# Optimization experiments

Hardware: AMD Instinct MI355X
Metric: run time of the kernel (lower is better)

Reference implementation:

```python
import jax, jax.numpy as jnp
import numpy as np

B, H, W, C, NC = 4, 64, 64, 64, 19


def setup_inputs() -> dict:
    key = jax.random.key(0)
    ks = jax.random.split(key, 12)
    s = 0.05  # small init so sigmoid scores are not saturated
    return {
        "feature": jax.random.normal(ks[0], (B, H, W, C), dtype=jnp.float32),
        "predict": jax.random.normal(ks[1], (B, H, W, NC), dtype=jnp.float32),
        # height attention params (dim = H); k_linear in source is unused (q reused as k)
        "hq_w": jax.random.normal(ks[2], (H, H), dtype=jnp.float32) * s,
        "hq_b": jnp.zeros((H,), dtype=jnp.float32),
        "hv_w": jax.random.normal(ks[3], (H, H), dtype=jnp.float32) * s,
        "hv_b": jnp.zeros((H,), dtype=jnp.float32),
        # width attention params (dim = W)
        "wq_w": jax.random.normal(ks[4], (W, W), dtype=jnp.float32) * s,
        "wq_b": jnp.zeros((W,), dtype=jnp.float32),
        "wv_w": jax.random.normal(ks[5], (W, W), dtype=jnp.float32) * s,
        "wv_b": jnp.zeros((W,), dtype=jnp.float32),
        # gating scalars (nn.Parameter(torch.zeros(1)) in source; random here to exercise path)
        "h_gate": jax.random.normal(ks[6], (1,), dtype=jnp.float32) * 0.5,
        "w_gate": jax.random.normal(ks[7], (1,), dtype=jnp.float32) * 0.5,
        # 1x1 conv num_classes -> 1 (stored as [NC, 1] matrix; 1x1 conv == per-pixel linear)
        "conv_w": jax.random.normal(ks[8], (NC, 1), dtype=jnp.float32) * s,
        "conv_b": jnp.zeros((1,), dtype=jnp.float32),
    }


def _self_atten(x, wq, bq, wv, bv, dim):
    # Source uses q_linear for BOTH q and k (k_linear dead), softmax replaced by sigmoid.
    q = x @ wq + bq                                   # [B, N, dim]
    v = x @ wv + bv                                   # [B, N, dim]
    scores = jax.nn.sigmoid(jnp.einsum('bnd,bmd->bnm', q, q) / jnp.sqrt(jnp.float32(dim)))
    return jnp.einsum('bnm,bmd->bnd', scores, v)      # [B, N, dim]


def _axial(x, hq_w, hq_b, hv_w, hv_b, wq_w, wq_b, wv_w, wv_b, h_gate, w_gate):
    b, h, w, c = x.shape
    # height attention: seq = W*C, feature dim = H
    xh = x.transpose(0, 2, 3, 1).reshape(b, w * c, h)
    xh = _self_atten(xh, hq_w, hq_b, hv_w, hv_b, h)
    xh = xh.reshape(b, w, c, h).transpose(0, 3, 1, 2)  # back to [B,H,W,C]
    x = xh * h_gate + x
    # width attention: seq = H*C, feature dim = W
    xw = x.transpose(0, 1, 3, 2).reshape(b, h * c, w)
    xw = _self_atten(xw, wq_w, wq_b, wv_w, wv_b, w)
    xw = xw.reshape(b, h, c, w).transpose(0, 1, 3, 2)  # back to [B,H,W,C]
    x = xw * w_gate + x
    return x


def reference(feature, predict, hq_w, hq_b, hv_w, hv_b, wq_w, wq_b, wv_w, wv_b,
              h_gate, w_gate, conv_w, conv_b):
    feat = feature + _axial(feature, hq_w, hq_b, hv_w, hv_b,
                            wq_w, wq_b, wv_w, wv_b, h_gate, w_gate)
    p = 1.0 - jax.nn.sigmoid(predict)                 # [B,H,W,NC]
    p = p @ conv_w + conv_b                           # 1x1 conv -> [B,H,W,1]
    return p * feat                                   # broadcast gate -> [B,H,W,C]
```

## Files before the change

### kernel.cpp

```cpp
#include <hip/hip_runtime.h>

typedef _Float16 f16x8 __attribute__((ext_vector_type(8)));
typedef __fp16   fp16x2 __attribute__((ext_vector_type(2)));
typedef float f32x16 __attribute__((ext_vector_type(16)));

__device__ __forceinline__ unsigned pkrtz(float a, float b) {
    fp16x2 h = __builtin_amdgcn_cvt_pkrtz(a, b);
    union { fp16x2 h; unsigned u; } c; c.h = h; return c.u;
}

__device__ __forceinline__ unsigned short f2h(float f) {
    _Float16 h = (_Float16)f;
    union { _Float16 h; unsigned short s; } c; c.h = h; return c.s;
}

__global__ __launch_bounds__(256) void prep_kernel(
    const float* __restrict__ src,
    const float* __restrict__ wq, const float* __restrict__ bq,
    const float* __restrict__ wv, const float* __restrict__ bv,
    unsigned short* __restrict__ Qg, unsigned short* __restrict__ Vtg)
{
    __shared__ float slab[64][65];
    __shared__ float wqs[4096];
    __shared__ float wvs[4096];

    const int t  = threadIdx.x;
    const int bx = blockIdx.x, b = blockIdx.y;

    {
        const float4* wq4 = (const float4*)wq;
        const float4* wv4 = (const float4*)wv;
        float4* q4 = (float4*)wqs; float4* v4 = (float4*)wvs;
        #pragma unroll
        for (int i = 0; i < 4; ++i) {
            q4[i*256 + t] = wq4[i*256 + t];
            v4[i*256 + t] = wv4[i*256 + t];
        }
    }
    {
        const int k = t >> 2, c0 = (t & 3) << 4;
        const size_t sb = (size_t)b*262144 + (size_t)k*4096 + (size_t)bx*64 + c0;
        #pragma unroll
        for (int i = 0; i < 4; ++i)
            *(float4*)&slab[k][c0 + i*4] = *(const float4*)&src[sb + i*4];
    }
    __syncthreads();

    const int c = t & 63, jg = t >> 6;
    float qa[16], va[16];
    #pragma unroll
    for (int jj = 0; jj < 16; ++jj) { qa[jj] = bq[jg*16+jj]; va[jj] = bv[jg*16+jj]; }
    for (int k = 0; k < 64; ++k) {
        const float xv = slab[k][c];
        const float* wqr = &wqs[k*64 + jg*16];
        const float* wvr = &wvs[k*64 + jg*16];
        #pragma unroll
        for (int jj = 0; jj < 16; ++jj) {
            qa[jj] += xv * wqr[jj];
            va[jj] += xv * wvr[jj];
        }
    }
    const int token = bx*64 + c;
    union { unsigned u[8]; uint4 v[2]; } qp;
    #pragma unroll
    for (int jj = 0; jj < 8; ++jj) qp.u[jj] = pkrtz(qa[2*jj], qa[2*jj+1]);
    const size_t qoff = ((size_t)b*4096 + token)*64 + jg*16;
    *(uint4*)&Qg[qoff]     = qp.v[0];
    *(uint4*)&Qg[qoff + 8] = qp.v[1];
    #pragma unroll
    for (int jj = 0; jj < 16; ++jj)
        Vtg[((size_t)b*64 + jg*16 + jj)*4096 + token] = f2h(va[jj]);
}

__global__ __launch_bounds__(256) void prep_w_kernel(
    const float* __restrict__ feature, const float* __restrict__ Pin,
    const float* __restrict__ gate,
    const float* __restrict__ wq, const float* __restrict__ bq,
    const float* __restrict__ wv, const float* __restrict__ bv,
    unsigned short* __restrict__ Qg, unsigned short* __restrict__ Vtg,
    float* __restrict__ x1out, int nsplit)
{
    __shared__ float slab[64][65];
    __shared__ float wqs[4096];
    __shared__ float wvs[4096];

    const int t  = threadIdx.x;
    const int bx = blockIdx.x, b = blockIdx.y;

    {
        const float4* wq4 = (const float4*)wq;
        const float4* wv4 = (const float4*)wv;
        float4* q4 = (float4*)wqs; float4* v4 = (float4*)wvs;
        #pragma unroll
        for (int i = 0; i < 4; ++i) {
            q4[i*256 + t] = wq4[i*256 + t];
            v4[i*256 + t] = wv4[i*256 + t];
        }
    }
    {
        const int k = t >> 2, c0 = (t & 3) << 4;
        const size_t off = (size_t)bx*4096 + (size_t)k*64 + c0;
        const size_t fb  = (size_t)b*262144 + off;
        const float g = gate[0];
        #pragma unroll
        for (int i = 0; i < 4; ++i) {
            float4 v  = *(const float4*)&feature[fb + i*4];
            float sx = 0.f, sy = 0.f, sz = 0.f, sw = 0.f;
            for (int ks = 0; ks < nsplit; ++ks) {
                float4 pk = *(const float4*)&Pin[((size_t)(ks*4 + b) << 18) + off + i*4];
                sx += pk.x; sy += pk.y; sz += pk.z; sw += pk.w;
            }
            v.x += g * sx; v.y += g * sy; v.z += g * sz; v.w += g * sw;
            *(float4*)&slab[k][c0 + i*4] = v;
            *(float4*)&x1out[fb + i*4] = v;
        }
    }
    __syncthreads();

    const int c = t & 63, jg = t >> 6;
    float qa[16], va[16];
    #pragma unroll
    for (int jj = 0; jj < 16; ++jj) { qa[jj] = bq[jg*16+jj]; va[jj] = bv[jg*16+jj]; }
    for (int k = 0; k < 64; ++k) {
        const float xv = slab[k][c];
        const float* wqr = &wqs[k*64 + jg*16];
        const float* wvr = &wvs[k*64 + jg*16];
        #pragma unroll
        for (int jj = 0; jj < 16; ++jj) {
            qa[jj] += xv * wqr[jj];
            va[jj] += xv * wvr[jj];
        }
    }
    const int token = bx*64 + c;
    union { unsigned u[8]; uint4 v[2]; } qp;
    #pragma unroll
    for (int jj = 0; jj < 8; ++jj) qp.u[jj] = pkrtz(qa[2*jj], qa[2*jj+1]);
    const size_t qoff = ((size_t)b*4096 + token)*64 + jg*16;
    *(uint4*)&Qg[qoff]     = qp.v[0];
    *(uint4*)&Qg[qoff + 8] = qp.v[1];
    #pragma unroll
    for (int jj = 0; jj < 16; ++jj)
        Vtg[((size_t)b*64 + jg*16 + jj)*4096 + token] = f2h(va[jj]);
}

__global__ __launch_bounds__(256) void attn_kernel(
    const unsigned short* __restrict__ Qg,
    const unsigned short* __restrict__ Vtg,
    float* __restrict__ P)
{
    __shared__ unsigned short Ksh[2][64][72];
    __shared__ unsigned short Vts[2][64][72];

    const int t = threadIdx.x;
    const int flat = blockIdx.x + 32*(blockIdx.y + 4*blockIdx.z);
    const int xcd  = flat & 7;
    const int slot = flat >> 3;
    const int mb   = slot & 31;
    const int grp  = xcd + ((slot >> 5) << 3);
    const int b      = grp >> 2;
    const int ksplit = grp & 3;
    const int niter = 16;
    const int keybase = ksplit * 1024;
    const int lane = t & 63, w = t >> 6;
    const int l32 = lane & 31, hi = lane >> 5;

    const unsigned short* Qbase = Qg  + (size_t)b*262144;
    const unsigned short* Vbase = Vtg + (size_t)b*262144;

    f16x8 qb[4];
    {
        const unsigned short* qrow = Qbase + (size_t)(mb*128 + w*32 + l32)*64 + hi*8;
        const _Float16 sc = (_Float16)(-0.180336880f);
        #pragma unroll
        for (int s = 0; s < 4; ++s) {
            f16x8 q = *(const f16x8*)(qrow + s*16);
            qb[s] = q * sc;
        }
    }

    f32x16 fz;
    #pragma unroll
    for (int i = 0; i < 16; ++i) fz[i] = 0.f;

    f32x16 y[2];
    y[0] = fz; y[1] = fz;

    const int lrow = t >> 2;
    const int loff = (t & 3) << 4;
    {
        const uint4* gk = (const uint4*)(Qbase + (size_t)(keybase + lrow)*64 + loff);
        uint4 k0 = gk[0], k1 = gk[1];
        const uint4* gv = (const uint4*)(Vbase + (size_t)lrow*4096 + keybase + loff);
        uint4 v0 = gv[0], v1 = gv[1];
        *(uint4*)&Ksh[0][lrow][loff]     = k0;
        *(uint4*)&Ksh[0][lrow][loff + 8] = k1;
        uint4 pa = { v0.x, v0.y, v1.x, v1.y };
        uint4 pb = { v0.z, v0.w, v1.z, v1.w };
        *(uint4*)&Vts[0][lrow][loff]     = pa;
        *(uint4*)&Vts[0][lrow][loff + 8] = pb;
    }
    __syncthreads();

    for (int kb = 0; kb < niter; ++kb) {
        const int cur = kb & 1, nxt = cur ^ 1;

        uint4 nk0 = {0,0,0,0}, nk1 = {0,0,0,0}, nv0 = {0,0,0,0}, nv1 = {0,0,0,0};
        if (kb < niter - 1) {
            const int keyn = keybase + (kb + 1)*64;
            const uint4* gk = (const uint4*)(Qbase + (size_t)(keyn + lrow)*64 + loff);
            nk0 = gk[0]; nk1 = gk[1];
            const uint4* gv = (const uint4*)(Vbase + (size_t)lrow*4096 + keyn + loff);
            nv0 = gv[0]; nv1 = gv[1];
        }

        f32x16 tt[2];
        #pragma unroll
        for (int s = 0; s < 4; ++s) {
            const int co = s*16 + hi*8;
            f16x8 ka0 = *(const f16x8*)&Ksh[cur][l32][co];
            f16x8 ka1 = *(const f16x8*)&Ksh[cur][32 + l32][co];
            if (s == 0) {
                tt[0] = __builtin_amdgcn_mfma_f32_32x32x16_f16(ka0, qb[0], fz, 0,0,0);
                tt[1] = __builtin_amdgcn_mfma_f32_32x32x16_f16(ka1, qb[0], fz, 0,0,0);
            } else {
                tt[0] = __builtin_amdgcn_mfma_f32_32x32x16_f16(ka0, qb[s], tt[0], 0,0,0);
                tt[1] = __builtin_amdgcn_mfma_f32_32x32x16_f16(ka1, qb[s], tt[1], 0,0,0);
            }
        }

        #pragma unroll
        for (int u = 0; u < 2; ++u) {
            unsigned pk_[8];
            #pragma unroll
            for (int pr = 0; pr < 8; ++pr) {
                float t0 = __builtin_fminf(tt[u][2*pr+0], 60.0f);
                float t1 = __builtin_fminf(tt[u][2*pr+1], 60.0f);
                float e0 = __builtin_exp2f(t0);
                float e1 = __builtin_exp2f(t1);
                float d0 = 1.0f + e0, d1 = 1.0f + e1;
                float rr = __builtin_amdgcn_rcpf(d0 * d1);
                pk_[pr] = pkrtz(rr * d1, rr * d0);
            }
            #pragma unroll
            for (int sp = 0; sp < 2; ++sp) {
                union { unsigned u4[4]; f16x8 v; } sa;
                sa.u4[0] = pk_[sp*4 + 0];
                sa.u4[1] = pk_[sp*4 + 1];
                sa.u4[2] = pk_[sp*4 + 2];
                sa.u4[3] = pk_[sp*4 + 3];
                const int ks = u*2 + sp;
                const int co = ks*16 + hi*8;
                f16x8 vb0 = *(const f16x8*)&Vts[cur][l32][co];
                f16x8 vb1 = *(const f16x8*)&Vts[cur][32 + l32][co];
                y[0] = __builtin_amdgcn_mfma_f32_32x32x16_f16(sa.v, vb0, y[0], 0,0,0);
                y[1] = __builtin_amdgcn_mfma_f32_32x32x16_f16(sa.v, vb1, y[1], 0,0,0);
            }
        }

        if (kb < niter - 1) {
            *(uint4*)&Ksh[nxt][lrow][loff]     = nk0;
            *(uint4*)&Ksh[nxt][lrow][loff + 8] = nk1;
            uint4 pa = { nv0.x, nv0.y, nv1.x, nv1.y };
            uint4 pb = { nv0.z, nv0.w, nv1.z, nv1.w };
            *(uint4*)&Vts[nxt][lrow][loff]     = pa;
            *(uint4*)&Vts[nxt][lrow][loff + 8] = pb;
        }
        __syncthreads();
    }

    float* Pp = P + (((size_t)(ksplit*4 + b)) << 18);
    const int token0 = mb*128 + w*32 + hi*4;
    #pragma unroll
    for (int dt = 0; dt < 2; ++dt) {
        const int d = dt*32 + l32;
        #pragma unroll
        for (int g = 0; g < 4; ++g) {
            float4 v;
            v.x = y[dt][4*g+0]; v.y = y[dt][4*g+1];
            v.z = y[dt][4*g+2]; v.w = y[dt][4*g+3];
            *(float4*)&Pp[(size_t)d*4096 + token0 + 8*g] = v;
        }
    }
}

__global__ __launch_bounds__(256) void final_kernel(
    const float* __restrict__ feature, const float* __restrict__ x1,
    const float* __restrict__ Pin, const float* __restrict__ predict,
    const float* __restrict__ conv_w, const float* __restrict__ conv_b,
    const float* __restrict__ gate, float* __restrict__ out, int nsplit)
{
    const int i4 = blockIdx.x * 256 + threadIdx.x;
    const int j = i4 << 2;
    const int pix = j >> 6;
    const float* row = predict + (size_t)pix * 19;
    float pv = conv_b[0];
    #pragma unroll
    for (int i = 0; i < 19; ++i) {
        float sg = __builtin_amdgcn_rcpf(1.0f + __builtin_exp2f(-1.442695041f * row[i]));
        pv += (1.0f - sg) * conv_w[i];
    }

    const int b = j >> 18, h = (j >> 12) & 63, d = (j >> 6) & 63, c = j & 63;
    const size_t pif = ((size_t)(b*64 + d) << 12) + h*64 + c;
    float sx = 0.f, sy = 0.f, sz = 0.f, sw = 0.f;
    for (int ks = 0; ks < nsplit; ++ks) {
        float4 pk = *(const float4*)&Pin[((size_t)ks << 20) + pif];
        sx += pk.x; sy += pk.y; sz += pk.z; sw += pk.w;
    }
    const float g = gate[0];
    float4 f = ((const float4*)feature)[i4];
    float4 x = ((const float4*)x1)[i4];
    float4 o;
    o.x = pv * (f.x + x.x + g * sx);
    o.y = pv * (f.y + x.y + g * sy);
    o.z = pv * (f.z + x.z + g * sz);
    o.w = pv * (f.w + x.w + g * sw);
    ((float4*)out)[i4] = o;
}

extern "C" void kernel_launch(void* const* d_in, const int* in_sizes, int n_in,
                              void* d_out, int out_size, void* d_ws, size_t ws_size,
                              hipStream_t stream) {
    const float* feature = (const float*)d_in[0];
    const float* predict = (const float*)d_in[1];
    const float* hq_w = (const float*)d_in[2];
    const float* hq_b = (const float*)d_in[3];
    const float* hv_w = (const float*)d_in[4];
    const float* hv_b = (const float*)d_in[5];
    const float* wq_w = (const float*)d_in[6];
    const float* wq_b = (const float*)d_in[7];
    const float* wv_w = (const float*)d_in[8];
    const float* wv_b = (const float*)d_in[9];
    const float* h_gate = (const float*)d_in[10];
    const float* w_gate = (const float*)d_in[11];
    const float* conv_w = (const float*)d_in[12];
    const float* conv_b = (const float*)d_in[13];
    float* out = (float*)d_out;

    char* ws = (char*)d_ws;
    unsigned short* Qg  = (unsigned short*)(ws);
    unsigned short* Vtg = (unsigned short*)(ws + (2u << 20));
    float*          x1  = (float*)(ws + (4u << 20));
    float*          P   = (float*)(ws + (8u << 20));
    const int nsplit = 4;

    dim3 blk(256);
    prep_kernel<<<dim3(64, 4), blk, 0, stream>>>(feature, hq_w, hq_b, hv_w, hv_b,
                                                 Qg, Vtg);
    attn_kernel<<<dim3(32, 4, 4), blk, 0, stream>>>(Qg, Vtg, P);
    prep_w_kernel<<<dim3(64, 4), blk, 0, stream>>>(feature, P, h_gate,
                                                   wq_w, wq_b, wv_w, wv_b,
                                                   Qg, Vtg, x1, nsplit);
    attn_kernel<<<dim3(32, 4, 4), blk, 0, stream>>>(Qg, Vtg, P);
    final_kernel<<<dim3(1024), blk, 0, stream>>>(feature, x1, P, predict,
                                                 conv_w, conv_b, w_gate, out, nsplit);
}
```

Baseline: 198.8 us.

## Process two query tiles per attention block to reuse K/V tiles

Each attention block now handles 256 query tokens (two 128-token tiles) instead of 128. Every K and V tile staged in shared memory is reused for both query tiles, and the grid is halved from 512 to 256 blocks. This cuts shared-memory loads and global K/V traffic per query. In exchange it roughly doubles the accumulator and fragment registers, which may lower occupancy, and with 256 blocks on a 256-CU part each CU gets about one block, so latency hiding comes only from within the block.

```diff
diff --git a/kernel.cpp b/kernel.cpp
--- a/kernel.cpp
+++ b/kernel.cpp
@@ -152,11 +152,11 @@
     __shared__ unsigned short Vts[2][64][72];
 
     const int t = threadIdx.x;
-    const int flat = blockIdx.x + 32*(blockIdx.y + 4*blockIdx.z);
+    const int flat = blockIdx.x + 16*(blockIdx.y + 4*blockIdx.z);
     const int xcd  = flat & 7;
     const int slot = flat >> 3;
-    const int mb   = slot & 31;
-    const int grp  = xcd + ((slot >> 5) << 3);
+    const int mb   = slot & 15;
+    const int grp  = xcd + ((slot >> 4) << 3);
     const int b      = grp >> 2;
     const int ksplit = grp & 3;
     const int niter = 16;
@@ -167,14 +167,17 @@
     const unsigned short* Qbase = Qg  + (size_t)b*262144;
     const unsigned short* Vbase = Vtg + (size_t)b*262144;
 
-    f16x8 qb[4];
-    {
-        const unsigned short* qrow = Qbase + (size_t)(mb*128 + w*32 + l32)*64 + hi*8;
+    f16x8 qfa[4], qfb[4];
+    {
+        const unsigned short* qrowA = Qbase + (size_t)(mb*256 + w*32 + l32)*64 + hi*8;
+        const unsigned short* qrowB = qrowA + 128*64;
         const _Float16 sc = (_Float16)(-0.180336880f);
         #pragma unroll
         for (int s = 0; s < 4; ++s) {
-            f16x8 q = *(const f16x8*)(qrow + s*16);
-            qb[s] = q * sc;
+            f16x8 qa = *(const f16x8*)(qrowA + s*16);
+            f16x8 qb = *(const f16x8*)(qrowB + s*16);
+            qfa[s] = qa * sc;
+            qfb[s] = qb * sc;
         }
     }
 
@@ -182,8 +185,8 @@
     #pragma unroll
     for (int i = 0; i < 16; ++i) fz[i] = 0.f;
 
-    f32x16 y[2];
-    y[0] = fz; y[1] = fz;
+    f32x16 ya[2], yb[2];
+    ya[0] = fz; ya[1] = fz; yb[0] = fz; yb[1] = fz;
 
     const int lrow = t >> 2;
     const int loff = (t & 3) << 4;
@@ -213,19 +216,36 @@
             nv0 = gv[0]; nv1 = gv[1];
         }
 
-        f32x16 tt[2];
+        f16x8 ka0[4], ka1[4];
         #pragma unroll
         for (int s = 0; s < 4; ++s) {
             const int co = s*16 + hi*8;
-            f16x8 ka0 = *(const f16x8*)&Ksh[cur][l32][co];
-            f16x8 ka1 = *(const f16x8*)&Ksh[cur][32 + l32][co];
+            ka0[s] = *(const f16x8*)&Ksh[cur][l32][co];
+            ka1[s] = *(const f16x8*)&Ksh[cur][32 + l32][co];
+        }
+
+        f32x16 ta[2], tb[2];
+        #pragma unroll
+        for (int s = 0; s < 4; ++s) {
             if (s == 0) {
-                tt[0] = __builtin_amdgcn_mfma_f32_32x32x16_f16(ka0, qb[0], fz, 0,0,0);
-                tt[1] = __builtin_amdgcn_mfma_f32_32x32x16_f16(ka1, qb[0], fz, 0,0,0);
+                ta[0] = __builtin_amdgcn_mfma_f32_32x32x16_f16(ka0[0], qfa[0], fz, 0,0,0);
+                ta[1] = __builtin_amdgcn_mfma_f32_32x32x16_f16(ka1[0], qfa[0], fz, 0,0,0);
+                tb[0] = __builtin_amdgcn_mfma_f32_32x32x16_f16(ka0[0], qfb[0], fz, 0,0,0);
+                tb[1] = __builtin_amdgcn_mfma_f32_32x32x16_f16(ka1[0], qfb[0], fz, 0,0,0);
             } else {
-                tt[0] = __builtin_amdgcn_mfma_f32_32x32x16_f16(ka0, qb[s], tt[0], 0,0,0);
-                tt[1] = __builtin_amdgcn_mfma_f32_32x32x16_f16(ka1, qb[s], tt[1], 0,0,0);
-            }
+                ta[0] = __builtin_amdgcn_mfma_f32_32x32x16_f16(ka0[s], qfa[s], ta[0], 0,0,0);
+                ta[1] = __builtin_amdgcn_mfma_f32_32x32x16_f16(ka1[s], qfa[s], ta[1], 0,0,0);
+                tb[0] = __builtin_amdgcn_mfma_f32_32x32x16_f16(ka0[s], qfb[s], tb[0], 0,0,0);
+                tb[1] = __builtin_amdgcn_mfma_f32_32x32x16_f16(ka1[s], qfb[s], tb[1], 0,0,0);
+            }
+        }
+
+        f16x8 vb0[4], vb1[4];
+        #pragma unroll
+        for (int ks = 0; ks < 4; ++ks) {
+            const int co = ks*16 + hi*8;
+            vb0[ks] = *(const f16x8*)&Vts[cur][l32][co];
+            vb1[ks] = *(const f16x8*)&Vts[cur][32 + l32][co];
         }
 
         #pragma unroll
@@ -233,8 +253,8 @@
             unsigned pk_[8];
             #pragma unroll
             for (int pr = 0; pr < 8; ++pr) {
-                float t0 = __builtin_fminf(tt[u][2*pr+0], 60.0f);
-                float t1 = __builtin_fminf(tt[u][2*pr+1], 60.0f);
+                float t0 = __builtin_fminf(ta[u][2*pr+0], 60.0f);
+                float t1 = __builtin_fminf(ta[u][2*pr+1], 60.0f);
                 float e0 = __builtin_exp2f(t0);
                 float e1 = __builtin_exp2f(t1);
                 float d0 = 1.0f + e0, d1 = 1.0f + e1;
@@ -249,11 +269,34 @@
                 sa.u4[2] = pk_[sp*4 + 2];
                 sa.u4[3] = pk_[sp*4 + 3];
                 const int ks = u*2 + sp;
-                const int co = ks*16 + hi*8;
-                f16x8 vb0 = *(const f16x8*)&Vts[cur][l32][co];
-                f16x8 vb1 = *(const f16x8*)&Vts[cur][32 + l32][co];
-                y[0] = __builtin_amdgcn_mfma_f32_32x32x16_f16(sa.v, vb0, y[0], 0,0,0);
-                y[1] = __builtin_amdgcn_mfma_f32_32x32x16_f16(sa.v, vb1, y[1], 0,0,0);
+                ya[0] = __builtin_amdgcn_mfma_f32_32x32x16_f16(sa.v, vb0[ks], ya[0], 0,0,0);
+                ya[1] = __builtin_amdgcn_mfma_f32_32x32x16_f16(sa.v, vb1[ks], ya[1], 0,0,0);
+            }
+        }
+
+        #pragma unroll
+        for (int u = 0; u < 2; ++u) {
+            unsigned pk_[8];
+            #pragma unroll
+            for (int pr = 0; pr < 8; ++pr) {
+                float t0 = __builtin_fminf(tb[u][2*pr+0], 60.0f);
+                float t1 = __builtin_fminf(tb[u][2*pr+1], 60.0f);
+                float e0 = __builtin_exp2f(t0);
+                float e1 = __builtin_exp2f(t1);
+                float d0 = 1.0f + e0, d1 = 1.0f + e1;
+                float rr = __builtin_amdgcn_rcpf(d0 * d1);
+                pk_[pr] = pkrtz(rr * d1, rr * d0);
+            }
+            #pragma unroll
+            for (int sp = 0; sp < 2; ++sp) {
+                union { unsigned u4[4]; f16x8 v; } sa;
+                sa.u4[0] = pk_[sp*4 + 0];
+                sa.u4[1] = pk_[sp*4 + 1];
+                sa.u4[2] = pk_[sp*4 + 2];
+                sa.u4[3] = pk_[sp*4 + 3];
+                const int ks = u*2 + sp;
+                yb[0] = __builtin_amdgcn_mfma_f32_32x32x16_f16(sa.v, vb0[ks], yb[0], 0,0,0);
+                yb[1] = __builtin_amdgcn_mfma_f32_32x32x16_f16(sa.v, vb1[ks], yb[1], 0,0,0);
             }
         }
 
@@ -269,16 +312,20 @@
     }
 
     float* Pp = P + (((size_t)(ksplit*4 + b)) << 18);
-    const int token0 = mb*128 + w*32 + hi*4;
+    const int token0 = mb*256 + w*32 + hi*4;
     #pragma unroll
     for (int dt = 0; dt < 2; ++dt) {
         const int d = dt*32 + l32;
         #pragma unroll
         for (int g = 0; g < 4; ++g) {
             float4 v;
-            v.x = y[dt][4*g+0]; v.y = y[dt][4*g+1];
-            v.z = y[dt][4*g+2]; v.w = y[dt][4*g+3];
+            v.x = ya[dt][4*g+0]; v.y = ya[dt][4*g+1];
+            v.z = ya[dt][4*g+2]; v.w = ya[dt][4*g+3];
             *(float4*)&Pp[(size_t)d*4096 + token0 + 8*g] = v;
+            float4 u;
+            u.x = yb[dt][4*g+0]; u.y = yb[dt][4*g+1];
+            u.z = yb[dt][4*g+2]; u.w = yb[dt][4*g+3];
+            *(float4*)&Pp[(size_t)d*4096 + token0 + 128 + 8*g] = u;
         }
     }
 }
@@ -347,11 +394,11 @@
     dim3 blk(256);
     prep_kernel<<<dim3(64, 4), blk, 0, stream>>>(feature, hq_w, hq_b, hv_w, hv_b,
                                                  Qg, Vtg);
-    attn_kernel<<<dim3(32, 4, 4), blk, 0, stream>>>(Qg, Vtg, P);
+    attn_kernel<<<dim3(16, 4, 4), blk, 0, stream>>>(Qg, Vtg, P);
     prep_w_kernel<<<dim3(64, 4), blk, 0, stream>>>(feature, P, h_gate,
                                                    wq_w, wq_b, wv_w, wv_b,
                                                    Qg, Vtg, x1, nsplit);
-    attn_kernel<<<dim3(32, 4, 4), blk, 0, stream>>>(Qg, Vtg, P);
+    attn_kernel<<<dim3(16, 4, 4), blk, 0, stream>>>(Qg, Vtg, P);
     final_kernel<<<dim3(1024), blk, 0, stream>>>(feature, x1, P, predict,
                                                  conv_w, conv_b, w_gate, out, nsplit);
 }
```

New measurement: 199.0 us. Within noise of the previous version (+0.1%).
